# Kernel tuning notes

Measured on AMD Instinct MI355X. Metric: run time of the kernel, lower is better.

The kernel has to match this reference:

```python
import jax, jax.numpy as jnp
import numpy as np

D_MODEL, D_INNER, D_STATE, D_CONV, DT_RANK = 512, 1024, 64, 4, 32
B, L = 2, 1000
EPS = 1e-5


def _rmsnorm(x, w):
    return x * jax.lax.rsqrt(jnp.mean(x * x, axis=-1, keepdims=True) + EPS) * w


def _causal_dwconv(x, w, b):
    # x: (B, L, Di); w: (Di, K) depthwise causal conv, output length L
    xT = jnp.transpose(x, (0, 2, 1))  # (B, Di, L)
    y = jax.lax.conv_general_dilated(
        xT, w[:, None, :], window_strides=(1,), padding=[(D_CONV - 1, 0)],
        dimension_numbers=('NCH', 'OIH', 'NCH'), feature_group_count=D_INNER)
    return jnp.transpose(y + b[None, :, None], (0, 2, 1))


def _selective_scan(u, dt, A, Bm, Cm):
    # u, dt: (B, L, Di); A: (Di, N); Bm, Cm: (B, L, N)
    def step(h, inp):
        dt_t, B_t, C_t, u_t = inp
        dA = jnp.exp(dt_t[..., None] * A)                       # (B, Di, N)
        h = dA * h + (dt_t * u_t)[..., None] * B_t[:, None, :]  # state update
        y = jnp.einsum('bdn,bn->bd', h, C_t)
        return h, y
    xs = (jnp.swapaxes(dt, 0, 1), jnp.swapaxes(Bm, 0, 1),
          jnp.swapaxes(Cm, 0, 1), jnp.swapaxes(u, 0, 1))
    h0 = jnp.zeros((u.shape[0], D_INNER, D_STATE), u.dtype)
    _, ys = jax.lax.scan(step, h0, xs)
    return jnp.swapaxes(ys, 0, 1)  # (B, L, Di)


def _mamba_layer(x, norm_w, in_proj, conv_w, conv_b, x_proj, dt_w, dt_b, A_log, Dp, out_proj):
    # mamba-ssm Block with fused_add_norm=False, n_layer=1:
    # residual = x; h = mixer(rmsnorm(x)); block output pair merges to h + x
    h = _rmsnorm(x, norm_w)
    xz = jnp.einsum('bld,ed->ble', h, in_proj)        # (B, L, 2*Di)
    xc, z = jnp.split(xz, 2, axis=-1)
    xc = jax.nn.silu(_causal_dwconv(xc, conv_w, conv_b))
    x_dbl = jnp.einsum('bld,ed->ble', xc, x_proj)     # (B, L, dt_rank + 2N)
    dt, Bm, Cm = jnp.split(x_dbl, [DT_RANK, DT_RANK + D_STATE], axis=-1)
    dt = jax.nn.softplus(jnp.einsum('blr,dr->bld', dt, dt_w) + dt_b)
    A = -jnp.exp(A_log)
    y = _selective_scan(xc, dt, A, Bm, Cm)
    y = (y + xc * Dp) * jax.nn.silu(z)
    return jnp.einsum('bld,ed->ble', y, out_proj) + x


def _forward(x,
             f_norm_w, f_in_proj, f_conv_w, f_conv_b, f_x_proj, f_dt_w, f_dt_b, f_A_log, f_D, f_out_proj,
             b_norm_w, b_in_proj, b_conv_w, b_conv_b, b_x_proj, b_dt_w, b_dt_b, b_A_log, b_D, b_out_proj):
    res_f = _mamba_layer(x, f_norm_w, f_in_proj, f_conv_w, f_conv_b, f_x_proj,
                         f_dt_w, f_dt_b, f_A_log, f_D, f_out_proj)
    res_b = _mamba_layer(jnp.flip(x, 1), b_norm_w, b_in_proj, b_conv_w, b_conv_b,
                         b_x_proj, b_dt_w, b_dt_b, b_A_log, b_D, b_out_proj)
    return res_f + jnp.flip(res_b, 1)  # bidirectional_merging='add'


def setup_inputs() -> dict:
    key = jax.random.key(0)
    ks = iter(jax.random.split(key, 32))
    def nrm(shape, s=0.02):
        return jax.random.normal(next(ks), shape, jnp.float32) * s
    inp = {'x': jax.random.normal(next(ks), (B, L, D_MODEL), jnp.float32)}
    for p in ('f', 'b'):
        inp[p + '_norm_w'] = jnp.ones((D_MODEL,), jnp.float32)
        inp[p + '_in_proj'] = nrm((2 * D_INNER, D_MODEL))
        inp[p + '_conv_w'] = nrm((D_INNER, D_CONV), 0.1)
        inp[p + '_conv_b'] = nrm((D_INNER,), 0.1)
        inp[p + '_x_proj'] = nrm((DT_RANK + 2 * D_STATE, D_INNER))
        inp[p + '_dt_w'] = nrm((D_INNER, DT_RANK), 0.1)
        inp[p + '_dt_b'] = jnp.full((D_INNER,), float(np.log(np.expm1(0.01))), jnp.float32)
        inp[p + '_A_log'] = jnp.log(jnp.tile(jnp.arange(1, D_STATE + 1, dtype=jnp.float32), (D_INNER, 1)))
        inp[p + '_D'] = jnp.ones((D_INNER,), jnp.float32)
        inp[p + '_out_proj'] = nrm((D_MODEL, D_INNER))
    return inp


def reference(x,
              f_norm_w, f_in_proj, f_conv_w, f_conv_b, f_x_proj, f_dt_w, f_dt_b, f_A_log, f_D, f_out_proj,
              b_norm_w, b_in_proj, b_conv_w, b_conv_b, b_x_proj, b_dt_w, b_dt_b, b_A_log, b_D, b_out_proj):
    return _forward(x,
                    f_norm_w, f_in_proj, f_conv_w, f_conv_b, f_x_proj, f_dt_w, f_dt_b, f_A_log, f_D, f_out_proj,
                    b_norm_w, b_in_proj, b_conv_w, b_conv_b, b_x_proj, b_dt_w, b_dt_b, b_A_log, b_D, b_out_proj)
```

## Files before the change

kernel.cpp:

```cpp
#include <hip/hip_runtime.h>
#include <hip/hip_bf16.h>
#include <math.h>

#define DM   512
#define DI   1024
#define NS   64
#define RDT  32
#define BB   2
#define LL   1000
#define MROWS (BB*LL)

typedef __attribute__((ext_vector_type(8))) short bf16x8;
typedef __attribute__((ext_vector_type(4))) float f32x4;

__device__ __forceinline__ unsigned short f2bf(float f) {
    unsigned u = __builtin_bit_cast(unsigned, f);
    u = (u + 0x7FFF + ((u >> 16) & 1)) >> 16;
    return (unsigned short)u;
}

__device__ __forceinline__ float bcast_lane(float v, int lane) {
    return __builtin_bit_cast(float,
        __builtin_amdgcn_readlane(__builtin_bit_cast(int, v), lane));
}

__global__ __launch_bounds__(256)
void rmsnorm_k(const float* __restrict__ x,
               const float* __restrict__ nw0, const float* __restrict__ nw1,
               unsigned short* __restrict__ xnb0, unsigned short* __restrict__ xnb1) {
    int row = blockIdx.x;
    int tid = threadIdx.x;
    const float* xr = x + (size_t)row * DM;
    float2 v = *(const float2*)(xr + tid * 2);
    float ss = v.x * v.x + v.y * v.y;
    #pragma unroll
    for (int off = 32; off; off >>= 1) ss += __shfl_xor(ss, off, 64);
    __shared__ float red[4];
    if ((tid & 63) == 0) red[tid >> 6] = ss;
    __syncthreads();
    float tot = red[0] + red[1] + red[2] + red[3];
    float scale = rsqrtf(tot / (float)DM + 1e-5f);
    float2 w0 = *(const float2*)(nw0 + tid * 2);
    float2 w1 = *(const float2*)(nw1 + tid * 2);
    short2 o0, o1;
    o0.x = (short)f2bf(v.x * scale * w0.x);
    o0.y = (short)f2bf(v.y * scale * w0.y);
    o1.x = (short)f2bf(v.x * scale * w1.x);
    o1.y = (short)f2bf(v.y * scale * w1.y);
    *(short2*)(xnb0 + (size_t)row * DM + tid * 2) = o0;
    *(short2*)(xnb1 + (size_t)row * DM + tid * 2) = o1;
}

__global__ __launch_bounds__(256)
void cvt_k(const float* __restrict__ in, unsigned short* __restrict__ out, int n4) {
    int idx = blockIdx.x * 256 + threadIdx.x;
    if (idx >= n4) return;
    float4 v = *(const float4*)(in + (size_t)idx * 4);
    short4 o;
    o.x = (short)f2bf(v.x); o.y = (short)f2bf(v.y);
    o.z = (short)f2bf(v.z); o.w = (short)f2bf(v.w);
    *(short4*)(out + (size_t)idx * 4) = o;
}

__global__ __launch_bounds__(256, 2)
void gemm1_mfma(const unsigned short* __restrict__ xnb0,
                const unsigned short* __restrict__ xnb1,
                const unsigned short* __restrict__ wib0,
                const unsigned short* __restrict__ wib1,
                float* __restrict__ xz0, float* __restrict__ xz1)
{
    __shared__ __align__(16) unsigned short As[128 * 40];
    __shared__ __align__(16) unsigned short Bs[128 * 40];
    int dir = blockIdx.z;
    const unsigned short* A = dir ? xnb1 : xnb0;
    const unsigned short* W = dir ? wib1 : wib0;
    float* C = dir ? xz1 : xz0;
    int n0 = blockIdx.x * 128, m0 = blockIdx.y * 128;
    int tid = threadIdx.x;
    int wv = tid >> 6, lane = tid & 63;
    int wr = wv >> 1, wc = wv & 1;
    int fl = lane & 15, kg = lane >> 4;

    f32x4 acc[4][4];
    #pragma unroll
    for (int i = 0; i < 4; i++)
        #pragma unroll
        for (int j = 0; j < 4; j++) acc[i][j] = (f32x4){0.f, 0.f, 0.f, 0.f};

    int sr = tid >> 2, cg = tid & 3;
    for (int k0 = 0; k0 < 512; k0 += 32) {
        #pragma unroll
        for (int i = 0; i < 2; i++) {
            int row = sr + i * 64;
            int m = m0 + row;
            float4 av = make_float4(0.f, 0.f, 0.f, 0.f);
            if (m < MROWS) {
                int rs = m;
                if (dir) { int b = m / LL, t = m % LL; rs = b * LL + (LL - 1 - t); }
                av = *(const float4*)(A + (size_t)rs * 512 + k0 + cg * 8);
            }
            *(float4*)(&As[row * 40 + cg * 8]) = av;
            float4 wv4 = *(const float4*)(W + (size_t)(n0 + row) * 512 + k0 + cg * 8);
            *(float4*)(&Bs[row * 40 + cg * 8]) = wv4;
        }
        __syncthreads();
        bf16x8 af[4], bf[4];
        #pragma unroll
        for (int fr = 0; fr < 4; fr++)
            af[fr] = *(const bf16x8*)(&As[(wr * 64 + fr * 16 + fl) * 40 + kg * 8]);
        #pragma unroll
        for (int fc = 0; fc < 4; fc++)
            bf[fc] = *(const bf16x8*)(&Bs[(wc * 64 + fc * 16 + fl) * 40 + kg * 8]);
        #pragma unroll
        for (int fr = 0; fr < 4; fr++)
            #pragma unroll
            for (int fc = 0; fc < 4; fc++)
                acc[fr][fc] = __builtin_amdgcn_mfma_f32_16x16x32_bf16(
                    af[fr], bf[fc], acc[fr][fc], 0, 0, 0);
        __syncthreads();
    }
    #pragma unroll
    for (int fr = 0; fr < 4; fr++)
        #pragma unroll
        for (int fc = 0; fc < 4; fc++)
            #pragma unroll
            for (int j = 0; j < 4; j++) {
                int m = m0 + wr * 64 + fr * 16 + kg * 4 + j;
                if (m < MROWS) {
                    int n = n0 + wc * 64 + fc * 16 + fl;
                    C[(size_t)m * 2048 + n] = acc[fr][fc][j];
                }
            }
}

__global__ __launch_bounds__(256, 2)
void gemm_out_mfma(const unsigned short* __restrict__ ygb0,
                   const unsigned short* __restrict__ ygb1,
                   const unsigned short* __restrict__ wob0,
                   const unsigned short* __restrict__ wob1,
                   float* __restrict__ partial)
{
    __shared__ __align__(16) unsigned short As[64 * 40];
    __shared__ __align__(16) unsigned short Bs[64 * 40];
    int z = blockIdx.z;
    int dir = z >> 1, ks = z & 1;
    const unsigned short* A = dir ? ygb1 : ygb0;
    const unsigned short* W = dir ? wob1 : wob0;
    float* P = partial + (size_t)z * MROWS * 512;
    int n0 = blockIdx.x * 64, m0 = blockIdx.y * 64;
    int kbase = ks * 512;
    int tid = threadIdx.x;
    int wv = tid >> 6, lane = tid & 63;
    int wr = wv >> 1, wc = wv & 1;
    int fl = lane & 15, kg = lane >> 4;

    f32x4 acc[2][2];
    #pragma unroll
    for (int i = 0; i < 2; i++)
        #pragma unroll
        for (int j = 0; j < 2; j++) acc[i][j] = (f32x4){0.f, 0.f, 0.f, 0.f};

    int sr = tid >> 2, cg = tid & 3;
    for (int k0 = 0; k0 < 512; k0 += 32) {
        int m = m0 + sr;
        float4 av = make_float4(0.f, 0.f, 0.f, 0.f);
        if (m < MROWS)
            av = *(const float4*)(A + (size_t)m * 1024 + kbase + k0 + cg * 8);
        *(float4*)(&As[sr * 40 + cg * 8]) = av;
        float4 wv4 = *(const float4*)(W + (size_t)(n0 + sr) * 1024 + kbase + k0 + cg * 8);
        *(float4*)(&Bs[sr * 40 + cg * 8]) = wv4;
        __syncthreads();
        bf16x8 af[2], bf[2];
        #pragma unroll
        for (int fr = 0; fr < 2; fr++)
            af[fr] = *(const bf16x8*)(&As[(wr * 32 + fr * 16 + fl) * 40 + kg * 8]);
        #pragma unroll
        for (int fc = 0; fc < 2; fc++)
            bf[fc] = *(const bf16x8*)(&Bs[(wc * 32 + fc * 16 + fl) * 40 + kg * 8]);
        #pragma unroll
        for (int fr = 0; fr < 2; fr++)
            #pragma unroll
            for (int fc = 0; fc < 2; fc++)
                acc[fr][fc] = __builtin_amdgcn_mfma_f32_16x16x32_bf16(
                    af[fr], bf[fc], acc[fr][fc], 0, 0, 0);
        __syncthreads();
    }
    #pragma unroll
    for (int fr = 0; fr < 2; fr++)
        #pragma unroll
        for (int fc = 0; fc < 2; fc++)
            #pragma unroll
            for (int j = 0; j < 4; j++) {
                int m = m0 + wr * 32 + fr * 16 + kg * 4 + j;
                if (m < MROWS) {
                    int n = n0 + wc * 32 + fc * 16 + fl;
                    P[(size_t)m * 512 + n] = acc[fr][fc][j];
                }
            }
}

__global__ __launch_bounds__(256)
void reduce_out_k(const float* __restrict__ x, const float* __restrict__ partial,
                  float* __restrict__ out)
{
    int idx = blockIdx.x * 256 + threadIdx.x;
    if (idx >= MROWS * 128) return;
    int m = idx >> 7, q = idx & 127;
    int b = m / LL, t = m % LL;
    int fm = b * LL + (LL - 1 - t);
    const float* p0 = partial;
    const float* p1 = partial + (size_t)MROWS * 512;
    const float* p2 = partial + (size_t)2 * MROWS * 512;
    const float* p3 = partial + (size_t)3 * MROWS * 512;
    float4 xv = *(const float4*)(x  + (size_t)m  * 512 + q * 4);
    float4 a  = *(const float4*)(p0 + (size_t)m  * 512 + q * 4);
    float4 bv = *(const float4*)(p1 + (size_t)m  * 512 + q * 4);
    float4 c  = *(const float4*)(p2 + (size_t)fm * 512 + q * 4);
    float4 d  = *(const float4*)(p3 + (size_t)fm * 512 + q * 4);
    float4 o;
    o.x = 2.f * xv.x + a.x + bv.x + c.x + d.x;
    o.y = 2.f * xv.y + a.y + bv.y + c.y + d.y;
    o.z = 2.f * xv.z + a.z + bv.z + c.z + d.z;
    o.w = 2.f * xv.w + a.w + bv.w + c.w + d.w;
    *(float4*)(out + (size_t)m * 512 + q * 4) = o;
}

__global__ __launch_bounds__(256)
void conv_silu_k(const float* __restrict__ xz0, const float* __restrict__ xz1,
                 const float* __restrict__ cw0, const float* __restrict__ cw1,
                 const float* __restrict__ cb0, const float* __restrict__ cb1,
                 float* __restrict__ xcT0, float* __restrict__ xcT1)
{
    __shared__ float Ls[64 * 65];
    int dirb = blockIdx.z;
    int dir = dirb >> 1, b = dirb & 1;
    int d0 = blockIdx.x * 64, t0 = blockIdx.y * 64;
    int tid = threadIdx.x;
    int dl = tid & 63, tg = tid >> 6;

    const float* in = (dir ? xz1 : xz0) + (size_t)b * LL * 2048;
    const float* cw = dir ? cw1 : cw0;
    const float* cb = dir ? cb1 : cb0;
    float*      xcT = dir ? xcT1 : xcT0;

    float4 w4 = ((const float4*)cw)[d0 + dl];
    float bias = cb[d0 + dl];

    int ts = t0 + tg * 16;
    float x3 = 0.f, x2 = 0.f, x1 = 0.f;
    if (ts - 3 >= 0 && ts - 3 < LL) x3 = in[(size_t)(ts - 3) * 2048 + d0 + dl];
    if (ts - 2 >= 0 && ts - 2 < LL) x2 = in[(size_t)(ts - 2) * 2048 + d0 + dl];
    if (ts - 1 >= 0 && ts - 1 < LL) x1 = in[(size_t)(ts - 1) * 2048 + d0 + dl];

    #pragma unroll
    for (int i = 0; i < 16; i++) {
        int t = ts + i;
        float x0v = (t < LL) ? in[(size_t)t * 2048 + d0 + dl] : 0.f;
        float a = bias + x3 * w4.x + x2 * w4.y + x1 * w4.z + x0v * w4.w;
        float s = a / (1.f + __expf(-a));
        Ls[dl * 65 + tg * 16 + i] = s;
        x3 = x2; x2 = x1; x1 = x0v;
    }
    __syncthreads();
    int tl = tid & 63, dg = tid >> 6;
    #pragma unroll
    for (int i = 0; i < 16; i++) {
        int dd = dg * 16 + i;
        int t = t0 + tl;
        if (t < LL)
            xcT[((size_t)(b * 1024) + d0 + dd) * LL + t] = Ls[dd * 65 + tl];
    }
}

__global__ __launch_bounds__(256)
void gemm_xp_k(const float* __restrict__ xcT0, const float* __restrict__ xcT1,
               const float* __restrict__ xp0, const float* __restrict__ xp1,
               float* __restrict__ xd0, float* __restrict__ xd1,
               float* __restrict__ bct)
{
    __shared__ float As[16 * 68];
    __shared__ float Ws[16 * 68];
    __shared__ float T[64 * 67];
    int dirb = blockIdx.z;
    int dir = dirb >> 1, b = dirb & 1;
    const float* xcT = (dir ? xcT1 : xcT0) + (size_t)b * 1024 * LL;
    const float* W   = dir ? xp1 : xp0;
    float*       C   = (dir ? xd1 : xd0) + (size_t)b * LL * 160;
    int n0 = blockIdx.x * 64, t0 = blockIdx.y * 64;
    int tid = threadIdx.x;
    int tx = tid & 15, ty = tid >> 4;

    float acc[4][4] = {};

    for (int k0 = 0; k0 < 1024; k0 += 16) {
        {
            int kk = tid & 15, mq = tid >> 4;
            float4 v = make_float4(0.f, 0.f, 0.f, 0.f);
            if (t0 + mq * 4 + 3 < LL)
                v = *(const float4*)(xcT + (size_t)(k0 + kk) * LL + t0 + mq * 4);
            *(float4*)(As + kk * 68 + mq * 4) = v;
        }
        {
            int row = tid >> 2, q = tid & 3;
            float4 v = make_float4(0.f, 0.f, 0.f, 0.f);
            if (n0 + row < 160)
                v = *(const float4*)(W + (size_t)(n0 + row) * 1024 + k0 + q * 4);
            Ws[(q * 4 + 0) * 68 + row] = v.x;
            Ws[(q * 4 + 1) * 68 + row] = v.y;
            Ws[(q * 4 + 2) * 68 + row] = v.z;
            Ws[(q * 4 + 3) * 68 + row] = v.w;
        }
        __syncthreads();
        #pragma unroll
        for (int k = 0; k < 16; k++) {
            float4 a = *(const float4*)(As + k * 68 + ty * 4);
            float4 w = *(const float4*)(Ws + k * 68 + tx * 4);
            float av[4] = {a.x, a.y, a.z, a.w};
            float wvv[4] = {w.x, w.y, w.z, w.w};
            #pragma unroll
            for (int i = 0; i < 4; i++)
                #pragma unroll
                for (int j = 0; j < 4; j++)
                    acc[i][j] = fmaf(av[i], wvv[j], acc[i][j]);
        }
        __syncthreads();
    }

    if (n0 == 0) {
        #pragma unroll
        for (int i = 0; i < 4; i++) {
            int t = t0 + ty * 4 + i;
            if (t >= LL) continue;
            #pragma unroll
            for (int j = 0; j < 4; j++) {
                int n = tx * 4 + j;
                C[(size_t)t * 160 + n] = acc[i][j];
            }
        }
    }

    #pragma unroll
    for (int i = 0; i < 4; i++)
        #pragma unroll
        for (int j = 0; j < 4; j++)
            T[(tx * 4 + j) * 67 + ty * 4 + i] = acc[i][j];
    __syncthreads();
    int tl = tid & 63, ng = tid >> 6;
    #pragma unroll
    for (int i = 0; i < 16; i++) {
        int nl = ng * 16 + i;
        int n = n0 + nl;
        int t = t0 + tl;
        if (n >= 32 && n < 160 && t < LL)
            bct[((size_t)dirb * 128 + (n - 32)) * LL + t] = T[nl * 67 + tl];
    }
}

__global__ __launch_bounds__(256)
void gemm_dt_k(const float* __restrict__ xd0, const float* __restrict__ xd1,
               const float* __restrict__ w0, const float* __restrict__ w1,
               const float* __restrict__ bb0, const float* __restrict__ bb1,
               float* __restrict__ dtT0, float* __restrict__ dtT1)
{
    __shared__ float As[64 * 33];
    __shared__ float Ws[32 * 68];
    __shared__ float T[64 * 67];
    int dirb = blockIdx.z;
    int dir = dirb >> 1, b = dirb & 1;
    const float* xd = (dir ? xd1 : xd0) + (size_t)b * LL * 160;
    const float* W  = dir ? w1 : w0;
    const float* bi = dir ? bb1 : bb0;
    float*      dtT = (dir ? dtT1 : dtT0) + (size_t)b * 1024 * LL;
    int n0 = blockIdx.x * 64, t0 = blockIdx.y * 64;
    int tid = threadIdx.x;
    int tx = tid & 15, ty = tid >> 4;

    #pragma unroll
    for (int i = 0; i < 2; i++) {
        int j = tid + 256 * i;
        int row = j >> 3, q = j & 7;
        float4 v = make_float4(0.f, 0.f, 0.f, 0.f);
        if (t0 + row < LL)
            v = *(const float4*)(xd + (size_t)(t0 + row) * 160 + q * 4);
        As[row * 33 + q * 4 + 0] = v.x;
        As[row * 33 + q * 4 + 1] = v.y;
        As[row * 33 + q * 4 + 2] = v.z;
        As[row * 33 + q * 4 + 3] = v.w;
        float4 wv = *(const float4*)(W + (size_t)(n0 + row) * 32 + q * 4);
        Ws[(q * 4 + 0) * 68 + row] = wv.x;
        Ws[(q * 4 + 1) * 68 + row] = wv.y;
        Ws[(q * 4 + 2) * 68 + row] = wv.z;
        Ws[(q * 4 + 3) * 68 + row] = wv.w;
    }
    __syncthreads();

    float acc[4][4] = {};
    #pragma unroll 8
    for (int k = 0; k < 32; k++) {
        float4 w = *(const float4*)(Ws + k * 68 + tx * 4);
        float wvv[4] = {w.x, w.y, w.z, w.w};
        float av[4];
        #pragma unroll
        for (int i = 0; i < 4; i++) av[i] = As[(ty * 4 + i) * 33 + k];
        #pragma unroll
        for (int i = 0; i < 4; i++)
            #pragma unroll
            for (int j = 0; j < 4; j++)
                acc[i][j] = fmaf(av[i], wvv[j], acc[i][j]);
    }
    __syncthreads();

    #pragma unroll
    for (int i = 0; i < 4; i++) {
        #pragma unroll
        for (int j = 0; j < 4; j++) {
            int n = tx * 4 + j;
            float v = acc[i][j] + bi[n0 + n];
            v = (v > 20.f) ? v : log1pf(__expf(v));
            T[n * 67 + ty * 4 + i] = v;
        }
    }
    __syncthreads();

    int tl = tid & 63, ng = tid >> 6;
    #pragma unroll
    for (int i = 0; i < 16; i++) {
        int nl = ng * 16 + i;
        int t = t0 + tl;
        if (t < LL)
            dtT[(size_t)(n0 + nl) * LL + t] = T[nl * 67 + tl];
    }
}

__global__ __launch_bounds__(256)
void scan_k(float* __restrict__ dtT0, float* __restrict__ dtT1,
            const float* __restrict__ ucT0, const float* __restrict__ ucT1,
            const float* __restrict__ bct,
            const float* __restrict__ Al0, const float* __restrict__ Al1,
            const float* __restrict__ Dc0, const float* __restrict__ Dc1)
{
    __shared__ float Bs[64 * 66];
    __shared__ float Cs[64 * 66];
    __shared__ float Pt[4][16 * 66];
    int dirb = blockIdx.y;
    int dir = dirb >> 1, b = dirb & 1;
    int wid = threadIdx.x >> 6, lane = threadIdx.x & 63;
    int d = blockIdx.x * 4 + wid;
    float* Pw = Pt[wid];

    float*       dtT = (dir ? dtT1 : dtT0);
    const float* ucT = (dir ? ucT1 : ucT0);
    const float* Al  = dir ? Al1 : Al0;
    const float* Dc  = dir ? Dc1 : Dc0;

    float a    = -__expf(Al[d * 64 + lane]) * 1.44269504f;
    float Dp64 = Dc[d] * (1.f / 64.f);
    float h    = 0.f;
    size_t chan = ((size_t)(b * 1024 + d)) * LL;
    const float* Bg = bct + (size_t)dirb * 128 * LL;

    int sr = threadIdx.x >> 4, c4 = (threadIdx.x & 15) * 4;
    int tl16 = lane & 15, qq = lane >> 4;
    const float* Prow = Pw + tl16 * 66 + qq * 16;

    for (int t0 = 0; t0 < LL; t0 += 64) {
        int rem = min(64, LL - t0);
        __syncthreads();
        #pragma unroll
        for (int i = 0; i < 4; i++) {
            int row = sr + i * 16;
            float4 bv = *(const float4*)(Bg + (size_t)row * LL + t0 + c4);
            float4 cv = *(const float4*)(Bg + (size_t)(row + 64) * LL + t0 + c4);
            *(float4*)(&Bs[row * 66 + c4]) = bv;
            *(float4*)(&Cs[row * 66 + c4]) = cv;
        }
        float dta = 0.f, ua = 0.f;
        if (lane < rem) {
            dta = dtT[chan + t0 + lane];
            ua  = ucT[chan + t0 + lane];
        }
        __syncthreads();

        for (int sec = 0; sec < 4; sec++) {
            int sbase = sec * 16;
            int steps = rem - sbase;
            if (steps <= 0) break;
            if (steps > 16) steps = 16;
            if (steps < 16) {
                for (int i = steps; i < 16; i++) Pw[i * 66 + lane] = 0.f;
            }
            int ngr = (steps + 7) >> 3;
            for (int g = 0; g < ngr; g++) {
                int tb = sbase + g * 8;
                float4 B0 = *(const float4*)(&Bs[lane * 66 + tb]);
                float4 B1 = *(const float4*)(&Bs[lane * 66 + tb + 4]);
                float4 C0 = *(const float4*)(&Cs[lane * 66 + tb]);
                float4 C1 = *(const float4*)(&Cs[lane * 66 + tb + 4]);
                #pragma unroll
                for (int i = 0; i < 8; i++) {
                    float dtv = bcast_lane(dta, tb + i);
                    float u   = bcast_lane(ua,  tb + i);
                    float dA  = exp2f(dtv * a);
                    float Bn  = (i < 4) ? B0[i] : B1[i - 4];
                    float Cn  = (i < 4) ? C0[i] : C1[i - 4];
                    h = fmaf(dA, h, dtv * u * Bn);
                    Pw[(g * 8 + i) * 66 + lane] = fmaf(u, Dp64, h * Cn);
                }
            }
            float s = 0.f;
            #pragma unroll
            for (int j = 0; j < 8; j++) {
                float2 v = *(const float2*)(Prow + j * 2);
                s += v.x + v.y;
            }
#if __has_builtin(__builtin_amdgcn_permlane32_swap)
            {
                unsigned aa = __builtin_bit_cast(unsigned, s);
                auto r = __builtin_amdgcn_permlane32_swap(aa, aa, false, false);
                s = __builtin_bit_cast(float, (unsigned)r[0]) +
                    __builtin_bit_cast(float, (unsigned)r[1]);
            }
#else
            s += __shfl_xor(s, 32, 64);
#endif
#if __has_builtin(__builtin_amdgcn_permlane16_swap)
            {
                unsigned aa = __builtin_bit_cast(unsigned, s);
                auto r = __builtin_amdgcn_permlane16_swap(aa, aa, false, false);
                s = __builtin_bit_cast(float, (unsigned)r[0]) +
                    __builtin_bit_cast(float, (unsigned)r[1]);
            }
#else
            s += __shfl_xor(s, 16, 64);
#endif
            if (lane < steps)
                dtT[chan + t0 + sbase + lane] = s;
        }
    }
}

__global__ __launch_bounds__(256)
void gate_k(const float* __restrict__ yT0, const float* __restrict__ yT1,
            float* __restrict__ xz0, float* __restrict__ xz1)
{
    __shared__ float Ls[64 * 65];
    int dirb = blockIdx.z;
    int dir = dirb >> 1, b = dirb & 1;
    int d0 = blockIdx.x * 64, t0 = blockIdx.y * 64;
    int tid = threadIdx.x;
    const float* yT = (dir ? yT1 : yT0) + (size_t)b * 1024 * LL;
    float*       xz = (dir ? xz1 : xz0) + (size_t)b * LL * 2048;

    int tl = tid & 63, dg = tid >> 6;
    #pragma unroll
    for (int i = 0; i < 16; i++) {
        int dd = dg * 16 + i;
        int t = t0 + tl;
        float v = (t < LL) ? yT[(size_t)(d0 + dd) * LL + t] : 0.f;
        Ls[dd * 65 + tl] = v;
    }
    __syncthreads();
    int dcol = tid & 63, tg = tid >> 6;
    #pragma unroll
    for (int i = 0; i < 16; i++) {
        int t = t0 + tg * 16 + i;
        if (t >= LL) continue;
        float z = xz[(size_t)t * 2048 + 1024 + d0 + dcol];
        float y = Ls[dcol * 65 + tg * 16 + i];
        float s = z / (1.f + __expf(-z));
        xz[(size_t)t * 2048 + d0 + dcol] = y * s;
    }
}

__global__ __launch_bounds__(256)
void cvt_yg_k(const float* __restrict__ xz0, const float* __restrict__ xz1,
              unsigned short* __restrict__ y0, unsigned short* __restrict__ y1)
{
    int idx = blockIdx.x * 256 + threadIdx.x;
    if (idx >= MROWS * 256) return;
    int dir = blockIdx.y;
    int t = idx >> 8, dq = idx & 255;
    const float* xz = dir ? xz1 : xz0;
    unsigned short* y = dir ? y1 : y0;
    float4 v = *(const float4*)(xz + (size_t)t * 2048 + dq * 4);
    short4 o;
    o.x = (short)f2bf(v.x); o.y = (short)f2bf(v.y);
    o.z = (short)f2bf(v.z); o.w = (short)f2bf(v.w);
    *(short4*)(y + (size_t)t * 1024 + dq * 4) = o;
}

extern "C" void kernel_launch(void* const* d_in, const int* in_sizes, int n_in,
                              void* d_out, int out_size, void* d_ws, size_t ws_size,
                              hipStream_t stream) {
    const float* x = (const float*)d_in[0];
    const float* P[2][10];
    for (int dir = 0; dir < 2; dir++)
        for (int i = 0; i < 10; i++)
            P[dir][i] = (const float*)d_in[1 + dir * 10 + i];

    float* ws = (float*)d_ws;
    float* xz0   = ws;
    float* xz1   = ws + 4096000;
    float* xcT0  = ws + 8192000;
    float* xcT1  = ws + 10240000;
    float* dtT0  = ws + 12288000;
    float* dtT1  = ws + 14336000;
    float* xdbl0 = ws + 16384000;
    float* xdbl1 = ws + 16704000;
    unsigned short* xnb0 = (unsigned short*)(ws + 17024000);
    unsigned short* xnb1 = (unsigned short*)(ws + 17280000);
    unsigned short* wib0 = (unsigned short*)dtT0;
    unsigned short* wib1 = (unsigned short*)dtT1;
    unsigned short* ygb0 = (unsigned short*)xcT0;
    unsigned short* ygb1 = (unsigned short*)xcT1;
    unsigned short* wob0 = (unsigned short*)dtT0;
    unsigned short* wob1 = (unsigned short*)dtT1;
    float* partial = xz0;
    float* bct = (float*)d_out;
    float* out = (float*)d_out;

    rmsnorm_k<<<MROWS, 256, 0, stream>>>(x, P[0][0], P[1][0], xnb0, xnb1);

    cvt_k<<<1024, 256, 0, stream>>>(P[0][1], wib0, 262144);
    cvt_k<<<1024, 256, 0, stream>>>(P[1][1], wib1, 262144);

    gemm1_mfma<<<dim3(16, 16, 2), 256, 0, stream>>>(
        xnb0, xnb1, wib0, wib1, xz0, xz1);

    conv_silu_k<<<dim3(16, 16, 4), 256, 0, stream>>>(
        xz0, xz1, P[0][2], P[1][2], P[0][3], P[1][3], xcT0, xcT1);

    gemm_xp_k<<<dim3(3, 16, 4), 256, 0, stream>>>(
        xcT0, xcT1, P[0][4], P[1][4], xdbl0, xdbl1, bct);

    gemm_dt_k<<<dim3(16, 16, 4), 256, 0, stream>>>(
        xdbl0, xdbl1, P[0][5], P[1][5], P[0][6], P[1][6], dtT0, dtT1);

    scan_k<<<dim3(256, 4), 256, 0, stream>>>(
        dtT0, dtT1, xcT0, xcT1, bct,
        P[0][7], P[1][7], P[0][8], P[1][8]);

    gate_k<<<dim3(16, 16, 4), 256, 0, stream>>>(
        dtT0, dtT1, xz0, xz1);

    cvt_yg_k<<<dim3(2000, 2), 256, 0, stream>>>(xz0, xz1, ygb0, ygb1);

    cvt_k<<<512, 256, 0, stream>>>(P[0][9], wob0, 131072);
    cvt_k<<<512, 256, 0, stream>>>(P[1][9], wob1, 131072);

    gemm_out_mfma<<<dim3(8, 32, 4), 256, 0, stream>>>(
        ygb0, ygb1, wob0, wob1, partial);

    reduce_out_k<<<1000, 256, 0, stream>>>(x, partial, out);
}
```

Before: 354.7 us.

## Fuse gate with bf16 conversion, drop out-proj split-K, shrink scan B/C tile

Gate kernel now writes bf16 gated output directly, removing the separate conversion pass and fp32 write-back. The output GEMM no longer splits K, so the reduction reads two partial buffers instead of four. Weight conversions per direction are merged into single launches, and the scan stages B/C in 32-step tiles instead of 64. Halving split-K reduces GEMM parallelism, and smaller scan tiles add more barriers per sequence.

```diff
diff --git a/kernel.cpp b/kernel.cpp
--- a/kernel.cpp
+++ b/kernel.cpp
@@ -52,9 +52,13 @@
 }
 
 __global__ __launch_bounds__(256)
-void cvt_k(const float* __restrict__ in, unsigned short* __restrict__ out, int n4) {
+void cvt2_k(const float* __restrict__ in0, const float* __restrict__ in1,
+            unsigned short* __restrict__ out0, unsigned short* __restrict__ out1,
+            int n4) {
     int idx = blockIdx.x * 256 + threadIdx.x;
     if (idx >= n4) return;
+    const float* in = blockIdx.y ? in1 : in0;
+    unsigned short* out = blockIdx.y ? out1 : out0;
     float4 v = *(const float4*)(in + (size_t)idx * 4);
     short4 o;
     o.x = (short)f2bf(v.x); o.y = (short)f2bf(v.y);
@@ -142,13 +146,11 @@
 {
     __shared__ __align__(16) unsigned short As[64 * 40];
     __shared__ __align__(16) unsigned short Bs[64 * 40];
-    int z = blockIdx.z;
-    int dir = z >> 1, ks = z & 1;
+    int dir = blockIdx.z;
     const unsigned short* A = dir ? ygb1 : ygb0;
     const unsigned short* W = dir ? wob1 : wob0;
-    float* P = partial + (size_t)z * MROWS * 512;
+    float* P = partial + (size_t)dir * MROWS * 512;
     int n0 = blockIdx.x * 64, m0 = blockIdx.y * 64;
-    int kbase = ks * 512;
     int tid = threadIdx.x;
     int wv = tid >> 6, lane = tid & 63;
     int wr = wv >> 1, wc = wv & 1;
@@ -161,13 +163,13 @@
         for (int j = 0; j < 2; j++) acc[i][j] = (f32x4){0.f, 0.f, 0.f, 0.f};
 
     int sr = tid >> 2, cg = tid & 3;
-    for (int k0 = 0; k0 < 512; k0 += 32) {
+    for (int k0 = 0; k0 < 1024; k0 += 32) {
         int m = m0 + sr;
         float4 av = make_float4(0.f, 0.f, 0.f, 0.f);
         if (m < MROWS)
-            av = *(const float4*)(A + (size_t)m * 1024 + kbase + k0 + cg * 8);
+            av = *(const float4*)(A + (size_t)m * 1024 + k0 + cg * 8);
         *(float4*)(&As[sr * 40 + cg * 8]) = av;
-        float4 wv4 = *(const float4*)(W + (size_t)(n0 + sr) * 1024 + kbase + k0 + cg * 8);
+        float4 wv4 = *(const float4*)(W + (size_t)(n0 + sr) * 1024 + k0 + cg * 8);
         *(float4*)(&Bs[sr * 40 + cg * 8]) = wv4;
         __syncthreads();
         bf16x8 af[2], bf[2];
@@ -210,18 +212,14 @@
     int fm = b * LL + (LL - 1 - t);
     const float* p0 = partial;
     const float* p1 = partial + (size_t)MROWS * 512;
-    const float* p2 = partial + (size_t)2 * MROWS * 512;
-    const float* p3 = partial + (size_t)3 * MROWS * 512;
     float4 xv = *(const float4*)(x  + (size_t)m  * 512 + q * 4);
     float4 a  = *(const float4*)(p0 + (size_t)m  * 512 + q * 4);
-    float4 bv = *(const float4*)(p1 + (size_t)m  * 512 + q * 4);
-    float4 c  = *(const float4*)(p2 + (size_t)fm * 512 + q * 4);
-    float4 d  = *(const float4*)(p3 + (size_t)fm * 512 + q * 4);
+    float4 c  = *(const float4*)(p1 + (size_t)fm * 512 + q * 4);
     float4 o;
-    o.x = 2.f * xv.x + a.x + bv.x + c.x + d.x;
-    o.y = 2.f * xv.y + a.y + bv.y + c.y + d.y;
-    o.z = 2.f * xv.z + a.z + bv.z + c.z + d.z;
-    o.w = 2.f * xv.w + a.w + bv.w + c.w + d.w;
+    o.x = 2.f * xv.x + a.x + c.x;
+    o.y = 2.f * xv.y + a.y + c.y;
+    o.z = 2.f * xv.z + a.z + c.z;
+    o.w = 2.f * xv.w + a.w + c.w;
     *(float4*)(out + (size_t)m * 512 + q * 4) = o;
 }
 
@@ -439,8 +437,8 @@
             const float* __restrict__ Al0, const float* __restrict__ Al1,
             const float* __restrict__ Dc0, const float* __restrict__ Dc1)
 {
-    __shared__ float Bs[64 * 66];
-    __shared__ float Cs[64 * 66];
+    __shared__ float Bs[64 * 34];
+    __shared__ float Cs[64 * 34];
     __shared__ float Pt[4][16 * 66];
     int dirb = blockIdx.y;
     int dir = dirb >> 1, b = dirb & 1;
@@ -459,20 +457,23 @@
     size_t chan = ((size_t)(b * 1024 + d)) * LL;
     const float* Bg = bct + (size_t)dirb * 128 * LL;
 
-    int sr = threadIdx.x >> 4, c4 = (threadIdx.x & 15) * 4;
+    int srow = threadIdx.x >> 2;
+    int scol = (threadIdx.x & 3) * 8;
     int tl16 = lane & 15, qq = lane >> 4;
     const float* Prow = Pw + tl16 * 66 + qq * 16;
 
-    for (int t0 = 0; t0 < LL; t0 += 64) {
-        int rem = min(64, LL - t0);
-        __syncthreads();
-        #pragma unroll
-        for (int i = 0; i < 4; i++) {
-            int row = sr + i * 16;
-            float4 bv = *(const float4*)(Bg + (size_t)row * LL + t0 + c4);
-            float4 cv = *(const float4*)(Bg + (size_t)(row + 64) * LL + t0 + c4);
-            *(float4*)(&Bs[row * 66 + c4]) = bv;
-            *(float4*)(&Cs[row * 66 + c4]) = cv;
+    for (int t0 = 0; t0 < LL; t0 += 32) {
+        int rem = min(32, LL - t0);
+        __syncthreads();
+        {
+            float4 b0 = *(const float4*)(Bg + (size_t)srow * LL + t0 + scol);
+            float4 b1 = *(const float4*)(Bg + (size_t)srow * LL + t0 + scol + 4);
+            float4 c0 = *(const float4*)(Bg + (size_t)(srow + 64) * LL + t0 + scol);
+            float4 c1 = *(const float4*)(Bg + (size_t)(srow + 64) * LL + t0 + scol + 4);
+            *(float4*)(&Bs[srow * 34 + scol])     = b0;
+            *(float4*)(&Bs[srow * 34 + scol + 4]) = b1;
+            *(float4*)(&Cs[srow * 34 + scol])     = c0;
+            *(float4*)(&Cs[srow * 34 + scol + 4]) = c1;
         }
         float dta = 0.f, ua = 0.f;
         if (lane < rem) {
@@ -481,7 +482,7 @@
         }
         __syncthreads();
 
-        for (int sec = 0; sec < 4; sec++) {
+        for (int sec = 0; sec < 2; sec++) {
             int sbase = sec * 16;
             int steps = rem - sbase;
             if (steps <= 0) break;
@@ -492,10 +493,10 @@
             int ngr = (steps + 7) >> 3;
             for (int g = 0; g < ngr; g++) {
                 int tb = sbase + g * 8;
-                float4 B0 = *(const float4*)(&Bs[lane * 66 + tb]);
-                float4 B1 = *(const float4*)(&Bs[lane * 66 + tb + 4]);
-                float4 C0 = *(const float4*)(&Cs[lane * 66 + tb]);
-                float4 C1 = *(const float4*)(&Cs[lane * 66 + tb + 4]);
+                float4 B0 = *(const float4*)(&Bs[lane * 34 + tb]);
+                float4 B1 = *(const float4*)(&Bs[lane * 34 + tb + 4]);
+                float4 C0 = *(const float4*)(&Cs[lane * 34 + tb]);
+                float4 C1 = *(const float4*)(&Cs[lane * 34 + tb + 4]);
                 #pragma unroll
                 for (int i = 0; i < 8; i++) {
                     float dtv = bcast_lane(dta, tb + i);
@@ -541,7 +542,8 @@
 
 __global__ __launch_bounds__(256)
 void gate_k(const float* __restrict__ yT0, const float* __restrict__ yT1,
-            float* __restrict__ xz0, float* __restrict__ xz1)
+            const float* __restrict__ xz0, const float* __restrict__ xz1,
+            unsigned short* __restrict__ yg0, unsigned short* __restrict__ yg1)
 {
     __shared__ float Ls[64 * 65];
     int dirb = blockIdx.z;
@@ -549,7 +551,8 @@
     int d0 = blockIdx.x * 64, t0 = blockIdx.y * 64;
     int tid = threadIdx.x;
     const float* yT = (dir ? yT1 : yT0) + (size_t)b * 1024 * LL;
-    float*       xz = (dir ? xz1 : xz0) + (size_t)b * LL * 2048;
+    const float* xz = (dir ? xz1 : xz0) + (size_t)b * LL * 2048;
+    unsigned short* yg = dir ? yg1 : yg0;
 
     int tl = tid & 63, dg = tid >> 6;
     #pragma unroll
@@ -568,25 +571,8 @@
         float z = xz[(size_t)t * 2048 + 1024 + d0 + dcol];
         float y = Ls[dcol * 65 + tg * 16 + i];
         float s = z / (1.f + __expf(-z));
-        xz[(size_t)t * 2048 + d0 + dcol] = y * s;
-    }
-}
-
-__global__ __launch_bounds__(256)
-void cvt_yg_k(const float* __restrict__ xz0, const float* __restrict__ xz1,
-              unsigned short* __restrict__ y0, unsigned short* __restrict__ y1)
-{
-    int idx = blockIdx.x * 256 + threadIdx.x;
-    if (idx >= MROWS * 256) return;
-    int dir = blockIdx.y;
-    int t = idx >> 8, dq = idx & 255;
-    const float* xz = dir ? xz1 : xz0;
-    unsigned short* y = dir ? y1 : y0;
-    float4 v = *(const float4*)(xz + (size_t)t * 2048 + dq * 4);
-    short4 o;
-    o.x = (short)f2bf(v.x); o.y = (short)f2bf(v.y);
-    o.z = (short)f2bf(v.z); o.w = (short)f2bf(v.w);
-    *(short4*)(y + (size_t)t * 1024 + dq * 4) = o;
+        yg[((size_t)(b * LL + t)) * 1024 + d0 + dcol] = f2bf(y * s);
+    }
 }
 
 extern "C" void kernel_launch(void* const* d_in, const int* in_sizes, int n_in,
@@ -621,8 +607,7 @@
 
     rmsnorm_k<<<MROWS, 256, 0, stream>>>(x, P[0][0], P[1][0], xnb0, xnb1);
 
-    cvt_k<<<1024, 256, 0, stream>>>(P[0][1], wib0, 262144);
-    cvt_k<<<1024, 256, 0, stream>>>(P[1][1], wib1, 262144);
+    cvt2_k<<<dim3(1024, 2), 256, 0, stream>>>(P[0][1], P[1][1], wib0, wib1, 262144);
 
     gemm1_mfma<<<dim3(16, 16, 2), 256, 0, stream>>>(
         xnb0, xnb1, wib0, wib1, xz0, xz1);
@@ -641,14 +626,11 @@
         P[0][7], P[1][7], P[0][8], P[1][8]);
 
     gate_k<<<dim3(16, 16, 4), 256, 0, stream>>>(
-        dtT0, dtT1, xz0, xz1);
-
-    cvt_yg_k<<<dim3(2000, 2), 256, 0, stream>>>(xz0, xz1, ygb0, ygb1);
-
-    cvt_k<<<512, 256, 0, stream>>>(P[0][9], wob0, 131072);
-    cvt_k<<<512, 256, 0, stream>>>(P[1][9], wob1, 131072);
-
-    gemm_out_mfma<<<dim3(8, 32, 4), 256, 0, stream>>>(
+        dtT0, dtT1, xz0, xz1, ygb0, ygb1);
+
+    cvt2_k<<<dim3(512, 2), 256, 0, stream>>>(P[0][9], P[1][9], wob0, wob1, 131072);
+
+    gemm_out_mfma<<<dim3(8, 32, 2), 256, 0, stream>>>(
         ygb0, ygb1, wob0, wob1, partial);
 
     reduce_out_k<<<1000, 256, 0, stream>>>(x, partial, out);
```

Result: faster. 335.1 us (-5.5%).
